# Performance work log

Measured on AMD Instinct MI355X. Metric: run time of the kernel, lower is better.

## Reference

```python
import jax, jax.numpy as jnp
import numpy as np


def setup_inputs() -> dict:
    key = jax.random.key(0)
    k1, k2 = jax.random.split(key)
    z = jax.random.normal(k1, (16, 256, 4096), dtype=jnp.float32)  # (B, z_dim, T)
    embedding = jax.random.normal(k2, (1024, 256), dtype=jnp.float32)  # (z_num, z_dim)
    return {"z": z, "embedding": embedding}


def reference(z, embedding):
    # z: (B, C, T) -> (B, T, C), matching z.transpose(1, 2)
    zt = jnp.transpose(z, (0, 2, 1))
    B, T, C = zt.shape
    z_flat = zt.reshape(-1, C)  # (N, C), N = B*T

    # squared-euclidean distances: ||z||^2 + ||e||^2 - 2 z e^T  -> (N, K)
    distances = (
        jnp.sum(z_flat * z_flat, axis=1, keepdims=True)
        + jnp.sum(embedding * embedding, axis=1)
        - 2.0 * z_flat @ embedding.T
    )
    encoding_idx = jnp.argmin(distances, axis=1)  # (N,)
    z_vq = embedding[encoding_idx].reshape(B, T, C)

    # perplexity of code usage (one-hot scatter -> mean)
    K = embedding.shape[0]
    counts = jnp.zeros((K,), dtype=jnp.float32).at[encoding_idx].add(1.0)
    avg_probs = counts / encoding_idx.shape[0]
    perplexity = jnp.exp(-jnp.sum(avg_probs * jnp.log(avg_probs + 1e-10)))

    # sparsity = cross_entropy(E E^T, arange) = mean(logsumexp(row) - diag)
    logits = embedding @ embedding.T  # (K, K)
    sparsity = jnp.mean(jax.nn.logsumexp(logits, axis=1) - jnp.diag(logits))

    sg = jax.lax.stop_gradient
    z_qut_loss = jnp.sum((z_vq - sg(zt)) ** 2)   # mse_loss reduction='sum'
    z_enc_loss = jnp.sum((sg(z_vq) - zt) ** 2)

    # straight-through estimator
    z_st = zt + sg(z_vq - zt)
    out = jnp.transpose(z_st, (0, 2, 1))  # back to (B, C, T)
    return (out, z_qut_loss, z_enc_loss, perplexity, sparsity)
```

## Files before the change

kernel.cpp:

```cpp
#include <hip/hip_runtime.h>
#include <math.h>

typedef unsigned int u32;
typedef unsigned long long u64;
typedef _Float16 f16x8 __attribute__((ext_vector_type(8)));
typedef _Float16 f16x4 __attribute__((ext_vector_type(4)));
typedef float f32x4 __attribute__((ext_vector_type(4)));
typedef __attribute__((address_space(1))) const char gch;
typedef __attribute__((address_space(3))) char lch;

#define ZD 256
#define KC 1024
#define TT 4096
#define BB 16
#define NROWS (BB*TT)
#define TAU 0.12f
#define FLAGCAP 32768

__device__ __forceinline__ u32 flip32(float s) {
    int i = __float_as_int(s);
    return (u32)(i ^ ((i >> 31) | 0x80000000));
}
__device__ __forceinline__ float unflip32(u32 u) {
    int m = (~(((int)u) >> 31)) | 0x80000000;
    return __int_as_float((int)(u ^ (u32)m));
}

__global__ __launch_bounds__(256)
void vq_prep_kernel(const float* __restrict__ emb, _Float16* __restrict__ eh,
                    float* __restrict__ re, int* __restrict__ cnt) {
    int gid = blockIdx.x * 256 + threadIdx.x;
    if (gid < 2) cnt[gid] = 0;

    int code = gid >> 6;
    int lane = threadIdx.x & 63;
    float4 v = *(const float4*)(emb + (size_t)code * ZD + lane * 4);
    float s = v.x*v.x + v.y*v.y + v.z*v.z + v.w*v.w;
    #pragma unroll
    for (int off = 32; off; off >>= 1) s += __shfl_down(s, off, 64);
    if (lane == 0) re[code] = s;

    f16x4 hv;
    hv[0] = (_Float16)v.x; hv[1] = (_Float16)v.y;
    hv[2] = (_Float16)v.z; hv[3] = (_Float16)v.w;
    *(f16x4*)(eh + (size_t)code * ZD + lane * 4) = hv;
}

__device__ __forceinline__ void stage_half8(const char* ehc, char* dstbase,
                                            int h, int w, int l) {
    const int srow = h * 16384;
    #pragma unroll
    for (int j = 0; j < 2; ++j) {
        const int gi  = w * 2 + j;
        const int c   = 2 * gi + (l >> 5);
        const int kbs = (l & 31) * 16;
        const int off = srow + c * 512 + (kbs ^ ((c & 7) << 4));
        __builtin_amdgcn_global_load_lds((gch*)(ehc + off),
                                         (lch*)(dstbase + gi * 1024), 16, 0, 0);
    }
}

__device__ __forceinline__ void compute_phase16(const char* hb, int h,
                                                const f16x8 (&ah)[8], const float* reL,
                                                float (&v1)[4], float (&v2)[4], int (&i1)[4],
                                                int lane15, int lk) {
    #pragma unroll
    for (int cg = 0; cg < 2; ++cg) {
        const int c  = cg * 16 + lane15;
        const int sw = (lane15 & 7) << 4;
        f16x8 bh[8];
        #pragma unroll
        for (int ks = 0; ks < 8; ++ks)
            bh[ks] = *(const f16x8*)(hb + c * 512 + ((lk * 16 + ks * 64) ^ sw));

        f32x4 ae = {0.f, 0.f, 0.f, 0.f};
        f32x4 ao = {0.f, 0.f, 0.f, 0.f};
        __builtin_amdgcn_s_setprio(1);
        #pragma unroll
        for (int ks = 0; ks < 4; ++ks) {
            ae = __builtin_amdgcn_mfma_f32_16x16x32_f16(ah[2 * ks],     bh[2 * ks],     ae, 0, 0, 0);
            ao = __builtin_amdgcn_mfma_f32_16x16x32_f16(ah[2 * ks + 1], bh[2 * ks + 1], ao, 0, 0, 0);
        }
        __builtin_amdgcn_s_setprio(0);

        const int codeg = h * 32 + c;
        const float rc = reL[codeg];
        #pragma unroll
        for (int r = 0; r < 4; ++r) {
            float s0 = fmaf(-2.f, ae[r] + ao[r], rc);
            float n2 = fminf(fmaxf(v1[r], s0), v2[r]);
            i1[r] = (s0 < v1[r]) ? codeg : i1[r];
            v1[r] = fminf(v1[r], s0);
            v2[r] = n2;
        }
    }
}

__global__ __launch_bounds__(512, 4)
void vq_argmin_mfma(const float* __restrict__ z, const _Float16* __restrict__ eh,
                    const float* __restrict__ emb, const float* __restrict__ re,
                    float* __restrict__ out, float* __restrict__ lossP,
                    int* __restrict__ idx, int* __restrict__ cnt,
                    int* __restrict__ flags) {
    __shared__ __align__(16) char lds[53248];
    float* reL    = (float*)(lds + 49152);
    int*   idsL   = (int*)lds;
    float* wlossL = (float*)(lds + 1024);

    const int tid = threadIdx.x;
    const int w   = tid >> 6;
    const int l   = tid & 63;
    const int lane15 = l & 15;
    const int lk     = l >> 4;
    const int r0  = blockIdx.x * 128;
    const int b   = r0 >> 12;
    const int t0  = r0 & 4095;
    const char* ehc = (const char*)eh;

    *(float2*)(reL + tid * 2) = *(const float2*)(re + tid * 2);

    f16x8 ah[8];
    float zsq = 0.f;
    {
        const char* zb = (const char*)(z + (size_t)b * ZD * TT + t0 + w * 16);
        char* zdst = lds + w * 4096;
        #pragma unroll
        for (int round = 0; round < 4; ++round) {
            #pragma unroll
            for (int j = 0; j < 4; ++j) {
                const int cl = j * 16 + (l >> 2);
                const int tb = (l & 3) * 16;
                const int c  = round * 64 + cl;
                const char* src = zb + (size_t)c * TT * 4 + tb;
                __builtin_amdgcn_global_load_lds((gch*)src, (lch*)(zdst + j * 1024),
                                                 16, 0, 0);
            }
            asm volatile("s_waitcnt vmcnt(0)" ::: "memory");
            __builtin_amdgcn_sched_barrier(0);
            #pragma unroll
            for (int ks2 = 0; ks2 < 2; ++ks2) {
                const int cl0 = ks2 * 32 + lk * 8;
                f16x8 h;
                #pragma unroll
                for (int j = 0; j < 8; ++j) {
                    float v = *(const float*)(zdst + (cl0 + j) * 64 + lane15 * 4);
                    zsq = fmaf(v, v, zsq);
                    h[j] = (_Float16)v;
                }
                ah[round * 2 + ks2] = h;
            }
            asm volatile("s_waitcnt lgkmcnt(0)" ::: "memory");
            __builtin_amdgcn_sched_barrier(0);
        }
    }
    zsq += __shfl_xor(zsq, 16, 64);
    zsq += __shfl_xor(zsq, 32, 64);

    float v1[4], v2[4];
    int   i1[4];
    #pragma unroll
    for (int r = 0; r < 4; ++r) { v1[r] = 3.4e38f; v2[r] = 3.4e38f; i1[r] = 0; }

    asm volatile("s_waitcnt vmcnt(0) lgkmcnt(0)" ::: "memory");
    __syncthreads();
    stage_half8(ehc, lds,         0, w, l);
    stage_half8(ehc, lds + 16384, 1, w, l);

    for (int h = 0; h < 31; ++h) {
        asm volatile("s_waitcnt vmcnt(2)" ::: "memory");
        __builtin_amdgcn_sched_barrier(0);
        __builtin_amdgcn_s_barrier();
        if (h < 30) stage_half8(ehc, lds + ((h + 2) % 3) * 16384, h + 2, w, l);
        compute_phase16(lds + (h % 3) * 16384, h, ah, reL, v1, v2, i1, lane15, lk);
    }
    asm volatile("s_waitcnt vmcnt(0)" ::: "memory");
    __builtin_amdgcn_sched_barrier(0);
    __builtin_amdgcn_s_barrier();
    compute_phase16(lds + (31 % 3) * 16384, 31, ah, reL, v1, v2, i1, lane15, lk);

    #pragma unroll
    for (int off = 1; off < 16; off <<= 1) {
        #pragma unroll
        for (int r = 0; r < 4; ++r) {
            float ov1 = __shfl_xor(v1[r], off, 64);
            int   oi1 = __shfl_xor(i1[r], off, 64);
            float ov2 = __shfl_xor(v2[r], off, 64);
            float nv2 = fminf(fmaxf(v1[r], ov1), fminf(v2[r], ov2));
            if (ov1 < v1[r] || (ov1 == v1[r] && oi1 < i1[r])) { v1[r] = ov1; i1[r] = oi1; }
            v2[r] = nv2;
        }
    }

    float zsr[4];
    #pragma unroll
    for (int r = 0; r < 4; ++r) zsr[r] = __shfl(zsq, lk * 4 + r, 64);

    __syncthreads();
    float lossw = 0.f;
    if (lane15 == 0) {
        #pragma unroll
        for (int r = 0; r < 4; ++r) {
            const int row = w * 16 + lk * 4 + r;
            idsL[row] = i1[r];
            const bool fl = (v2[r] - v1[r] < TAU);
            lossw += fl ? zsr[r] : (zsr[r] + v1[r]);
            if (fl) {
                int p = atomicAdd(cnt, 1);
                if (p < FLAGCAP) flags[p] = (r0 + row) | (i1[r] << 16);
            }
        }
    }
    lossw += __shfl_xor(lossw, 16, 64);
    lossw += __shfl_xor(lossw, 32, 64);
    if (l == 0) wlossL[w] = lossw;
    __syncthreads();

    if (tid < 128) idx[r0 + tid] = idsL[tid];
    if (tid == 0) {
        float s = 0.f;
        #pragma unroll
        for (int j = 0; j < 8; ++j) s += wlossL[j];
        lossP[blockIdx.x] = s;
    }

    {
        const int c0 = w * 32;
        float* ob = out + (size_t)b * ZD * TT + t0;
        #pragma unroll
        for (int half = 0; half < 2; ++half) {
            const int tt = half * 64 + l;
            const int ii = idsL[tt];
            const float4* er4 = (const float4*)(emb + (size_t)ii * ZD + c0);
            #pragma unroll
            for (int c4 = 0; c4 < 8; ++c4) {
                float4 ev = er4[c4];
                float* o0 = ob + (size_t)(c0 + c4 * 4) * TT + tt;
                o0[0]      = ev.x;
                o0[TT]     = ev.y;
                o0[2 * TT] = ev.z;
                o0[3 * TT] = ev.w;
            }
        }
    }
}

__global__ __launch_bounds__(1024)
void vq_fixspar(const float* __restrict__ z, const float* __restrict__ emb,
                const float* __restrict__ re, const int* __restrict__ cnt,
                const int* __restrict__ flags, float* __restrict__ out,
                int* __restrict__ idx, float* __restrict__ sparLse,
                float* __restrict__ addP) {
    const int tid = threadIdx.x;
    const int w   = tid >> 6;
    const int lane = tid & 63;

    if (blockIdx.x >= 256) {
        __shared__ __align__(16) float er[8][260];
        __shared__ float wmaxS[8][16];
        __shared__ float wsumS[8][16];
        const int sb = blockIdx.x - 256;
        const int r0 = sb * 8;

        for (int i = tid; i < 8 * 256; i += 1024) er[i >> 8][i & 255] = emb[(size_t)r0 * ZD + i];
        __syncthreads();

        const int c = tid;
        const float4* ec = (const float4*)(emb + (size_t)c * ZD);
        float a[8] = {0.f,0.f,0.f,0.f,0.f,0.f,0.f,0.f};
        #pragma unroll 4
        for (int k4 = 0; k4 < ZD / 4; ++k4) {
            float4 e4 = ec[k4];
            #pragma unroll
            for (int r = 0; r < 8; ++r) {
                const float* a4 = &er[r][k4 * 4];
                a[r] = fmaf(e4.x, a4[0], fmaf(e4.y, a4[1],
                       fmaf(e4.z, a4[2], fmaf(e4.w, a4[3], a[r]))));
            }
        }
        #pragma unroll
        for (int r = 0; r < 8; ++r) {
            float m = a[r];
            #pragma unroll
            for (int off = 32; off; off >>= 1) m = fmaxf(m, __shfl_xor(m, off, 64));
            if (lane == 0) wmaxS[r][w] = m;
        }
        __syncthreads();
        float M[8];
        #pragma unroll
        for (int r = 0; r < 8; ++r) {
            float m = wmaxS[r][0];
            #pragma unroll
            for (int j = 1; j < 16; ++j) m = fmaxf(m, wmaxS[r][j]);
            M[r] = m;
            float se = expf(a[r] - m);
            #pragma unroll
            for (int off = 32; off; off >>= 1) se += __shfl_xor(se, off, 64);
            if (lane == 0) wsumS[r][w] = se;
        }
        __syncthreads();
        if (tid < 8) {
            float S = 0.f;
            #pragma unroll
            for (int j = 0; j < 16; ++j) S += wsumS[tid][j];
            sparLse[r0 + tid] = M[tid] + logf(S);
        }
        return;
    }

    __shared__ __align__(16) float zs[8][ZD];
    __shared__ u64 sb2[16][8];
    __shared__ int nwS[8];
    __shared__ float addS;
    int n = cnt[0];
    if (n > FLAGCAP) n = FLAGCAP;
    float blkLoss = 0.f;

    const int c = tid;
    const float4* ec = (const float4*)(emb + (size_t)c * ZD);
    const float rc = re[c];

    for (int base = blockIdx.x * 8; base < n; base += 256 * 8) {
        const int nr = (n - base < 8) ? (n - base) : 8;
        __syncthreads();
        for (int i = tid; i < nr * 256; i += 1024) {
            const int r = i >> 8, k = i & 255;
            const int rowg = flags[base + r] & 0xFFFF;
            zs[r][k] = z[(size_t)(rowg >> 12) * ZD * TT + (size_t)k * TT + (rowg & 4095)];
        }
        __syncthreads();

        float a[8] = {0.f,0.f,0.f,0.f,0.f,0.f,0.f,0.f};
        #pragma unroll 4
        for (int k4 = 0; k4 < ZD / 4; ++k4) {
            float4 e4 = ec[k4];
            #pragma unroll
            for (int r = 0; r < 8; ++r) {
                const float* a4 = &zs[r][k4 * 4];
                a[r] = fmaf(e4.x, a4[0], fmaf(e4.y, a4[1],
                       fmaf(e4.z, a4[2], fmaf(e4.w, a4[3], a[r]))));
            }
        }
        #pragma unroll
        for (int r = 0; r < 8; ++r) {
            if (r < nr) {
                float s = fmaf(-2.f, a[r], rc);
                u64 bv = ((u64)flip32(s) << 32) | (u32)c;
                #pragma unroll
                for (int off = 32; off; off >>= 1) {
                    u64 o = (u64)__shfl_xor((long long)bv, off, 64);
                    if (o < bv) bv = o;
                }
                if (lane == 0) sb2[w][r] = bv;
            }
        }
        __syncthreads();
        if (tid == 0) addS = 0.f;
        __syncthreads();
        if (tid < nr) {
            u64 m = sb2[0][tid];
            #pragma unroll
            for (int j = 1; j < 16; ++j) if (sb2[j][tid] < m) m = sb2[j][tid];
            const int nc  = (int)(u32)(m & 0xFFFFFFFFull);
            const float s = unflip32((u32)(m >> 32));
            const int rowg = flags[base + tid] & 0xFFFF;
            const int old  = (flags[base + tid] >> 16) & 1023;
            atomicAdd(&addS, s);
            if (nc != old) { idx[rowg] = nc; nwS[tid] = nc; }
            else nwS[tid] = -1;
        }
        __syncthreads();
        if (tid == 0) blkLoss += addS;
        for (int r = 0; r < nr; ++r) {
            const int nw = nwS[r];
            if (nw >= 0 && tid < 256) {
                const int rowg = flags[base + r] & 0xFFFF;
                out[(size_t)(rowg >> 12) * ZD * TT + (size_t)tid * TT + (rowg & 4095)]
                    = emb[(size_t)nw * ZD + tid];
            }
        }
    }
    if (tid == 0) addP[blockIdx.x] = blkLoss;
}

__global__ __launch_bounds__(1024)
void vq_final_kernel(const int* __restrict__ idx, const float* __restrict__ re,
                     const float* __restrict__ sparLse, const float* __restrict__ lossP,
                     const float* __restrict__ addP, float* __restrict__ scal) {
    __shared__ int   histL[4][1024];
    __shared__ float red[1024];
    const int tid = threadIdx.x;
    const int g   = tid >> 8;

    histL[0][tid] = 0; histL[1][tid] = 0; histL[2][tid] = 0; histL[3][tid] = 0;
    __syncthreads();
    #pragma unroll 4
    for (int i = 0; i < 64; ++i)
        atomicAdd(&histL[g][idx[i * 1024 + tid]], 1);
    __syncthreads();
    const int hc = histL[0][tid] + histL[1][tid] + histL[2][tid] + histL[3][tid];
    float p = (float)hc * (1.0f / (float)NROWS);
    red[tid] = -p * logf(p + 1e-10f);
    __syncthreads();
    for (int st = 512; st; st >>= 1) {
        if (tid < st) red[tid] += red[tid + st];
        __syncthreads();
    }
    if (tid == 0) scal[2] = expf(red[0]);
    __syncthreads();

    red[tid] = (tid < 512 ? lossP[tid] : 0.f) + ((tid < 256) ? addP[tid] : 0.f);
    __syncthreads();
    for (int st = 512; st; st >>= 1) {
        if (tid < st) red[tid] += red[tid + st];
        __syncthreads();
    }
    if (tid == 0) { scal[0] = red[0]; scal[1] = red[0]; }
    __syncthreads();

    red[tid] = sparLse[tid] - re[tid];
    __syncthreads();
    for (int st = 512; st; st >>= 1) {
        if (tid < st) red[tid] += red[tid + st];
        __syncthreads();
    }
    if (tid == 0) scal[3] = red[0] * (1.0f / (float)KC);
}

extern "C" void kernel_launch(void* const* d_in, const int* in_sizes, int n_in,
                              void* d_out, int out_size, void* d_ws, size_t ws_size,
                              hipStream_t stream) {
    const float* z   = (const float*)d_in[0];
    const float* emb = (const float*)d_in[1];
    float* out = (float*)d_out;
    const size_t NOUT = (size_t)BB * ZD * TT;
    float* scal = out + NOUT;

    float* re      = (float*)d_ws;
    int*   cnt     = (int*)(re + KC);
    int*   flags   = cnt + 4;
    float* sparLse = (float*)(flags + FLAGCAP);
    float* lossP   = sparLse + KC;
    float* addP    = lossP + 512;
    int*   idx     = (int*)(addP + 256);
    _Float16* eh   = (_Float16*)(idx + NROWS);

    vq_prep_kernel<<<256, 256, 0, stream>>>(emb, eh, re, cnt);
    vq_argmin_mfma<<<NROWS / 128, 512, 0, stream>>>(z, eh, emb, re, out, lossP, idx,
                                                    cnt, flags);
    vq_fixspar<<<384, 1024, 0, stream>>>(z, emb, re, cnt, flags, out, idx,
                                         sparLse, addP);
    vq_final_kernel<<<1, 1024, 0, stream>>>(idx, re, sparLse, lossP, addP, scal);
}
```

Before: 142.8 us.

## Split codebook across wave halves so each B tile feeds two row groups

Reorganizes the argmin GEMM work split. Before, each of 8 waves owned 16 rows and scanned all 1024 codes. Now each wave owns 32 rows (two A fragments) and scans half the codebook, so each LDS-loaded B fragment feeds two MFMAs, halving LDS B reads per MFMA. The two code halves are merged through LDS at the end. This costs more registers for A fragments and accumulators, extra block-wide syncs in the z staging, and a cross-half merge step.

```diff
diff --git a/kernel.cpp b/kernel.cpp
--- a/kernel.cpp
+++ b/kernel.cpp
@@ -46,53 +46,54 @@
     *(f16x4*)(eh + (size_t)code * ZD + lane * 4) = hv;
 }
 
-__device__ __forceinline__ void stage_half8(const char* ehc, char* dstbase,
-                                            int h, int w, int l) {
-    const int srow = h * 16384;
+__device__ __forceinline__ void stage_tile16(const char* ehc_h, char* dstbase,
+                                             int h, int wr, int l) {
+    const int srow = h * 8192;
     #pragma unroll
     for (int j = 0; j < 2; ++j) {
-        const int gi  = w * 2 + j;
+        const int gi  = wr * 2 + j;
         const int c   = 2 * gi + (l >> 5);
         const int kbs = (l & 31) * 16;
         const int off = srow + c * 512 + (kbs ^ ((c & 7) << 4));
-        __builtin_amdgcn_global_load_lds((gch*)(ehc + off),
+        __builtin_amdgcn_global_load_lds((gch*)(ehc_h + off),
                                          (lch*)(dstbase + gi * 1024), 16, 0, 0);
     }
 }
 
-__device__ __forceinline__ void compute_phase16(const char* hb, int h,
-                                                const f16x8 (&ah)[8], const float* reL,
-                                                float (&v1)[4], float (&v2)[4], int (&i1)[4],
-                                                int lane15, int lk) {
-    #pragma unroll
-    for (int cg = 0; cg < 2; ++cg) {
-        const int c  = cg * 16 + lane15;
-        const int sw = (lane15 & 7) << 4;
-        f16x8 bh[8];
-        #pragma unroll
-        for (int ks = 0; ks < 8; ++ks)
-            bh[ks] = *(const f16x8*)(hb + c * 512 + ((lk * 16 + ks * 64) ^ sw));
-
-        f32x4 ae = {0.f, 0.f, 0.f, 0.f};
-        f32x4 ao = {0.f, 0.f, 0.f, 0.f};
-        __builtin_amdgcn_s_setprio(1);
-        #pragma unroll
-        for (int ks = 0; ks < 4; ++ks) {
-            ae = __builtin_amdgcn_mfma_f32_16x16x32_f16(ah[2 * ks],     bh[2 * ks],     ae, 0, 0, 0);
-            ao = __builtin_amdgcn_mfma_f32_16x16x32_f16(ah[2 * ks + 1], bh[2 * ks + 1], ao, 0, 0, 0);
-        }
-        __builtin_amdgcn_s_setprio(0);
-
-        const int codeg = h * 32 + c;
-        const float rc = reL[codeg];
-        #pragma unroll
-        for (int r = 0; r < 4; ++r) {
-            float s0 = fmaf(-2.f, ae[r] + ao[r], rc);
-            float n2 = fminf(fmaxf(v1[r], s0), v2[r]);
-            i1[r] = (s0 < v1[r]) ? codeg : i1[r];
-            v1[r] = fminf(v1[r], s0);
-            v2[r] = n2;
-        }
+__device__ __forceinline__ void compute16(const char* tb, int codeg0,
+                                          const f16x8 (&ah)[2][8], const float* reL,
+                                          float (&v1)[8], float (&v2)[8], int (&i1)[8],
+                                          int lane15, int lk) {
+    const int sw = (lane15 & 7) << 4;
+    f16x8 bh[8];
+    #pragma unroll
+    for (int ks = 0; ks < 8; ++ks)
+        bh[ks] = *(const f16x8*)(tb + lane15 * 512 + ((lk * 16 + ks * 64) ^ sw));
+
+    f32x4 a0 = {0.f, 0.f, 0.f, 0.f};
+    f32x4 a1 = {0.f, 0.f, 0.f, 0.f};
+    __builtin_amdgcn_s_setprio(1);
+    #pragma unroll
+    for (int ks = 0; ks < 8; ++ks) {
+        a0 = __builtin_amdgcn_mfma_f32_16x16x32_f16(ah[0][ks], bh[ks], a0, 0, 0, 0);
+        a1 = __builtin_amdgcn_mfma_f32_16x16x32_f16(ah[1][ks], bh[ks], a1, 0, 0, 0);
+    }
+    __builtin_amdgcn_s_setprio(0);
+
+    const int codeg = codeg0 + lane15;
+    const float rc = reL[codeg];
+    #pragma unroll
+    for (int r = 0; r < 4; ++r) {
+        float s0 = fmaf(-2.f, a0[r], rc);
+        float n2a = fminf(fmaxf(v1[r], s0), v2[r]);
+        i1[r] = (s0 < v1[r]) ? codeg : i1[r];
+        v1[r] = fminf(v1[r], s0);
+        v2[r] = n2a;
+        float s1 = fmaf(-2.f, a1[r], rc);
+        float n2b = fminf(fmaxf(v1[4 + r], s1), v2[4 + r]);
+        i1[4 + r] = (s1 < v1[4 + r]) ? codeg : i1[4 + r];
+        v1[4 + r] = fminf(v1[4 + r], s1);
+        v2[4 + r] = n2b;
     }
 }
 
@@ -102,126 +103,147 @@
                     float* __restrict__ out, float* __restrict__ lossP,
                     int* __restrict__ idx, int* __restrict__ cnt,
                     int* __restrict__ flags) {
-    __shared__ __align__(16) char lds[53248];
-    float* reL    = (float*)(lds + 49152);
+    __shared__ __align__(16) char lds[53760];
+    float* reL  = (float*)(lds + 49152);
+    float* zsqL = (float*)(lds + 53248);
     int*   idsL   = (int*)lds;
-    float* wlossL = (float*)(lds + 1024);
+    float* wlossL = (float*)(lds + 512);
+    float* v1h    = (float*)(lds + 1024);
+    float* v2h    = (float*)(lds + 2048);
+    int*   i1h    = (int*)(lds + 3072);
 
     const int tid = threadIdx.x;
     const int w   = tid >> 6;
     const int l   = tid & 63;
     const int lane15 = l & 15;
     const int lk     = l >> 4;
+    const int hf  = w >> 2;
+    const int wr  = w & 3;
     const int r0  = blockIdx.x * 128;
     const int b   = r0 >> 12;
     const int t0  = r0 & 4095;
-    const char* ehc = (const char*)eh;
+    const char* ehc_h = (const char*)eh + (size_t)hf * 512 * 512;
 
     *(float2*)(reL + tid * 2) = *(const float2*)(re + tid * 2);
 
-    f16x8 ah[8];
-    float zsq = 0.f;
+    f16x8 ah[2][8];
+    float zsq[2] = {0.f, 0.f};
     {
-        const char* zb = (const char*)(z + (size_t)b * ZD * TT + t0 + w * 16);
-        char* zdst = lds + w * 4096;
+        const char* zb = (const char*)(z + (size_t)b * ZD * TT + t0);
         #pragma unroll
         for (int round = 0; round < 4; ++round) {
             #pragma unroll
             for (int j = 0; j < 4; ++j) {
-                const int cl = j * 16 + (l >> 2);
-                const int tb = (l & 3) * 16;
-                const int c  = round * 64 + cl;
-                const char* src = zb + (size_t)c * TT * 4 + tb;
-                __builtin_amdgcn_global_load_lds((gch*)src, (lch*)(zdst + j * 1024),
-                                                 16, 0, 0);
+                const int chunk = w * 4 + j;
+                const int c  = round * 64 + chunk * 2 + (l >> 5);
+                const char* src = zb + ((size_t)c * TT + (l & 31) * 4) * 4;
+                __builtin_amdgcn_global_load_lds((gch*)src,
+                                                 (lch*)(lds + chunk * 1024), 16, 0, 0);
             }
             asm volatile("s_waitcnt vmcnt(0)" ::: "memory");
             __builtin_amdgcn_sched_barrier(0);
-            #pragma unroll
-            for (int ks2 = 0; ks2 < 2; ++ks2) {
-                const int cl0 = ks2 * 32 + lk * 8;
-                f16x8 h;
+            __syncthreads();
+            #pragma unroll
+            for (int rg = 0; rg < 2; ++rg) {
+                const int t_loc = wr * 32 + rg * 16 + lane15;
                 #pragma unroll
-                for (int j = 0; j < 8; ++j) {
-                    float v = *(const float*)(zdst + (cl0 + j) * 64 + lane15 * 4);
-                    zsq = fmaf(v, v, zsq);
-                    h[j] = (_Float16)v;
+                for (int ks2 = 0; ks2 < 2; ++ks2) {
+                    const int cl0 = ks2 * 32 + lk * 8;
+                    f16x8 h;
+                    #pragma unroll
+                    for (int j = 0; j < 8; ++j) {
+                        float v = *(const float*)(lds + (cl0 + j) * 512 + t_loc * 4);
+                        zsq[rg] = fmaf(v, v, zsq[rg]);
+                        h[j] = (_Float16)v;
+                    }
+                    ah[rg][round * 2 + ks2] = h;
                 }
-                ah[round * 2 + ks2] = h;
-            }
-            asm volatile("s_waitcnt lgkmcnt(0)" ::: "memory");
-            __builtin_amdgcn_sched_barrier(0);
-        }
-    }
-    zsq += __shfl_xor(zsq, 16, 64);
-    zsq += __shfl_xor(zsq, 32, 64);
-
-    float v1[4], v2[4];
-    int   i1[4];
-    #pragma unroll
-    for (int r = 0; r < 4; ++r) { v1[r] = 3.4e38f; v2[r] = 3.4e38f; i1[r] = 0; }
+            }
+            __syncthreads();
+        }
+    }
+    #pragma unroll
+    for (int rg = 0; rg < 2; ++rg) {
+        zsq[rg] += __shfl_xor(zsq[rg], 16, 64);
+        zsq[rg] += __shfl_xor(zsq[rg], 32, 64);
+    }
+    if (hf == 0 && l < 16) {
+        zsqL[wr * 32 + l]      = zsq[0];
+        zsqL[wr * 32 + 16 + l] = zsq[1];
+    }
+
+    float v1[8], v2[8];
+    int   i1[8];
+    #pragma unroll
+    for (int s8 = 0; s8 < 8; ++s8) { v1[s8] = 3.4e38f; v2[s8] = 3.4e38f; i1[s8] = 0; }
 
     asm volatile("s_waitcnt vmcnt(0) lgkmcnt(0)" ::: "memory");
     __syncthreads();
-    stage_half8(ehc, lds,         0, w, l);
-    stage_half8(ehc, lds + 16384, 1, w, l);
-
+    char* ring = lds + hf * 24576;
+    stage_tile16(ehc_h, ring,        0, wr, l);
+    stage_tile16(ehc_h, ring + 8192, 1, wr, l);
+
+    const int cbase = hf * 512;
     for (int h = 0; h < 31; ++h) {
         asm volatile("s_waitcnt vmcnt(2)" ::: "memory");
         __builtin_amdgcn_sched_barrier(0);
         __builtin_amdgcn_s_barrier();
-        if (h < 30) stage_half8(ehc, lds + ((h + 2) % 3) * 16384, h + 2, w, l);
-        compute_phase16(lds + (h % 3) * 16384, h, ah, reL, v1, v2, i1, lane15, lk);
+        if (h < 30) stage_tile16(ehc_h, ring + ((h + 2) % 3) * 8192, h + 2, wr, l);
+        compute16(ring + (h % 3) * 8192, cbase + h * 16, ah, reL, v1, v2, i1, lane15, lk);
     }
     asm volatile("s_waitcnt vmcnt(0)" ::: "memory");
     __builtin_amdgcn_sched_barrier(0);
     __builtin_amdgcn_s_barrier();
-    compute_phase16(lds + (31 % 3) * 16384, 31, ah, reL, v1, v2, i1, lane15, lk);
+    compute16(ring + (31 % 3) * 8192, cbase + 31 * 16, ah, reL, v1, v2, i1, lane15, lk);
 
     #pragma unroll
     for (int off = 1; off < 16; off <<= 1) {
         #pragma unroll
-        for (int r = 0; r < 4; ++r) {
-            float ov1 = __shfl_xor(v1[r], off, 64);
-            int   oi1 = __shfl_xor(i1[r], off, 64);
-            float ov2 = __shfl_xor(v2[r], off, 64);
-            float nv2 = fminf(fmaxf(v1[r], ov1), fminf(v2[r], ov2));
-            if (ov1 < v1[r] || (ov1 == v1[r] && oi1 < i1[r])) { v1[r] = ov1; i1[r] = oi1; }
-            v2[r] = nv2;
-        }
-    }
-
-    float zsr[4];
-    #pragma unroll
-    for (int r = 0; r < 4; ++r) zsr[r] = __shfl(zsq, lk * 4 + r, 64);
-
-    __syncthreads();
-    float lossw = 0.f;
+        for (int s8 = 0; s8 < 8; ++s8) {
+            float ov1 = __shfl_xor(v1[s8], off, 64);
+            int   oi1 = __shfl_xor(i1[s8], off, 64);
+            float ov2 = __shfl_xor(v2[s8], off, 64);
+            float nv2 = fminf(fmaxf(v1[s8], ov1), fminf(v2[s8], ov2));
+            if (ov1 < v1[s8] || (ov1 == v1[s8] && oi1 < i1[s8])) { v1[s8] = ov1; i1[s8] = oi1; }
+            v2[s8] = nv2;
+        }
+    }
+
+    __syncthreads();
     if (lane15 == 0) {
         #pragma unroll
-        for (int r = 0; r < 4; ++r) {
-            const int row = w * 16 + lk * 4 + r;
-            idsL[row] = i1[r];
-            const bool fl = (v2[r] - v1[r] < TAU);
-            lossw += fl ? zsr[r] : (zsr[r] + v1[r]);
-            if (fl) {
-                int p = atomicAdd(cnt, 1);
-                if (p < FLAGCAP) flags[p] = (r0 + row) | (i1[r] << 16);
-            }
-        }
-    }
-    lossw += __shfl_xor(lossw, 16, 64);
-    lossw += __shfl_xor(lossw, 32, 64);
-    if (l == 0) wlossL[w] = lossw;
-    __syncthreads();
-
-    if (tid < 128) idx[r0 + tid] = idsL[tid];
-    if (tid == 0) {
-        float s = 0.f;
-        #pragma unroll
-        for (int j = 0; j < 8; ++j) s += wlossL[j];
-        lossP[blockIdx.x] = s;
-    }
+        for (int s8 = 0; s8 < 8; ++s8) {
+            const int rg = s8 >> 2, rr = s8 & 3;
+            const int row = wr * 32 + rg * 16 + lk * 4 + rr;
+            v1h[hf * 128 + row] = v1[s8];
+            v2h[hf * 128 + row] = v2[s8];
+            i1h[hf * 128 + row] = i1[s8];
+        }
+    }
+    __syncthreads();
+
+    if (tid < 128) {
+        const float va1 = v1h[tid], vb1 = v1h[128 + tid];
+        const float va2 = v2h[tid], vb2 = v2h[128 + tid];
+        const int   ia1 = i1h[tid], ib1 = i1h[128 + tid];
+        float nv1; int ni1;
+        if (vb1 < va1) { nv1 = vb1; ni1 = ib1; }
+        else           { nv1 = va1; ni1 = ia1; }
+        const float nv2 = fminf(fmaxf(va1, vb1), fminf(va2, vb2));
+        idsL[tid] = ni1;
+        idx[r0 + tid] = ni1;
+        const bool fl = (nv2 - nv1 < TAU);
+        float lv = fl ? zsqL[tid] : (zsqL[tid] + nv1);
+        if (fl) {
+            int p = atomicAdd(cnt, 1);
+            if (p < FLAGCAP) flags[p] = (r0 + tid) | (ni1 << 16);
+        }
+        #pragma unroll
+        for (int off = 32; off; off >>= 1) lv += __shfl_down(lv, off, 64);
+        if (l == 0) wlossL[tid >> 6] = lv;
+    }
+    __syncthreads();
+    if (tid == 0) lossP[blockIdx.x] = wlossL[0] + wlossL[1];
 
     {
         const int c0 = w * 32;
```

Measured after the change: 216.6 us. 1.52x slower.
